# Performance work log

Hardware: AMD Instinct MI355X
Metric: run time of the kernel (lower is better)

Reference implementation:

```python
import jax, jax.numpy as jnp
import numpy as np

B, S, H = 8, 4096, 512

def setup_inputs() -> dict:
    key = jax.random.key(0)
    k1, k2 = jax.random.split(key)
    lstm_out = jax.random.normal(k1, (B, S, H), dtype=jnp.float32)
    W = jax.random.normal(k2, (2 * H, H), dtype=jnp.float32) * (1.0 / np.sqrt(H))
    b = jnp.zeros((2 * H,), dtype=jnp.float32)
    return {"lstm_out": lstm_out, "W": W, "b": b}

def reference(lstm_out, W, b):
    # noise_net: Linear(H, 2H) + Softplus
    noise = jax.nn.softplus(jnp.einsum('bsh,oh->bso', lstm_out, W) + b)  # [B,S,2H]
    Q = noise[:, :, :H]   # process noise
    R = noise[:, :, H:]   # observation noise

    def step(carry, inp):
        state, P = carry
        z, q, r = inp                      # each [B,H]
        P_pred = P + q
        K = P_pred / (P_pred + r + 1e-6)
        state = state + K * (z - state)
        P = (1.0 - K) * P_pred
        return (state, P), state

    state0 = lstm_out[:, 0, :]
    P0 = jnp.full_like(state0, 0.1)
    # time-major for scan: [S,B,H]
    xs = (jnp.swapaxes(lstm_out, 0, 1),
          jnp.swapaxes(Q, 0, 1),
          jnp.swapaxes(R, 0, 1))
    _, states = jax.lax.scan(step, (state0, P0), xs)  # [S,B,H]
    return jnp.swapaxes(states, 0, 1)  # [B,S,H]
```

## Files before the change

### kernel.cpp

```cpp
#include <hip/hip_runtime.h>
#include <hip/hip_bf16.h>

#define B_ 8
#define S_ 4096
#define H_ 512

using short8 = __attribute__((ext_vector_type(8))) short;
using f32x4  = __attribute__((ext_vector_type(4))) float;

__device__ __forceinline__ float bf2f(unsigned u16) {
    return __uint_as_float(u16 << 16);
}
__device__ __forceinline__ unsigned pk2bf(float x, float y) {
    __hip_bfloat162 h = __float22bfloat162_rn(make_float2(x, y));
    return *reinterpret_cast<unsigned*>(&h);
}
__device__ __forceinline__ float softplus_f(float x) {
    float sp = __logf(1.0f + __expf(x));
    return x > 15.0f ? x : sp;
}

typedef __attribute__((address_space(1))) void* gbl_ptr_t;
typedef __attribute__((address_space(3))) void* lds_ptr_t;
__device__ __forceinline__ void gload_lds16(const void* g, void* l) {
    __builtin_amdgcn_global_load_lds((gbl_ptr_t)g, (lds_ptr_t)l, 16, 0, 0);
}

#define ASZ8 2097152u
#define TOT8 2162688u

__global__ __launch_bounds__(256)
void convert_bf16(const float* __restrict__ A, const float* __restrict__ Wm,
                  uint4* __restrict__ Ab, uint4* __restrict__ Wb) {
    unsigned i = blockIdx.x * 256u + threadIdx.x;
    const float4* src; uint4* dst; unsigned off;
    if (i < ASZ8) { src = (const float4*)A;  dst = Ab; off = i; }
    else          { src = (const float4*)Wm; dst = Wb; off = i - ASZ8; }
    float4 a = src[2u * off], b = src[2u * off + 1u];
    uint4 o;
    o.x = pk2bf(a.x, a.y); o.y = pk2bf(a.z, a.w);
    o.z = pk2bf(b.x, b.y); o.w = pk2bf(b.z, b.w);
    dst[off] = o;
}

#define TM 128
#define TN 128
#define BK 64

__global__ __launch_bounds__(256)
void gemm_softplus(const unsigned short* __restrict__ Ab,
                   const unsigned short* __restrict__ Wb,
                   const float* __restrict__ bias,
                   unsigned* __restrict__ QR) {
    __shared__ unsigned short As[TM * BK];
    __shared__ unsigned short Bs[TN * BK];

    const int bid     = blockIdx.x;
    const int logical = (bid & 7) * 256 + (bid >> 3);
    const int bm = logical >> 3;
    const int bn = logical & 7;

    const int t    = threadIdx.x;
    const int wave = t >> 6;
    const int lane = t & 63;
    const int wm  = (wave >> 1) * 64;
    const int wn  = (wave & 1) * 64;
    const int l15 = lane & 15;
    const int l4  = lane >> 4;

    const int m0 = bm * TM;

    const int lr = lane >> 3;
    const int su = ((lane & 7) ^ lr) * 8;

    f32x4 acc[4][4] = {};

    for (int kc = 0; kc < 512; kc += BK) {
#pragma unroll
        for (int i = 0; i < 4; ++i) {
            const int j   = wave * 4 + i;
            const int row = j * 8 + lr;
            gload_lds16(Ab + (size_t)(m0 + row) * 512 + kc + su, &As[j * 512]);
            const int n = bn * 64 + (row & 31) + ((row & 64) >> 1) + ((row & 32) << 4);
            gload_lds16(Wb + (size_t)n * 512 + kc + su, &Bs[j * 512]);
        }
        __syncthreads();

#pragma unroll
        for (int kk = 0; kk < 2; ++kk) {
            short8 af[4], bf[4];
#pragma unroll
            for (int i = 0; i < 4; ++i) {
                const int ra = wm + i * 16 + l15;
                const int ua = ((kk * 4 + l4) ^ (ra & 7)) * 8;
                af[i] = *(const short8*)&As[ra * 64 + ua];
                const int rb = wn + i * 16 + l15;
                const int ub = ((kk * 4 + l4) ^ (rb & 7)) * 8;
                bf[i] = *(const short8*)&Bs[rb * 64 + ub];
            }
#pragma unroll
            for (int i = 0; i < 4; ++i)
#pragma unroll
                for (int j = 0; j < 4; ++j)
                    acc[i][j] = __builtin_amdgcn_mfma_f32_16x16x32_bf16(af[i], bf[j], acc[i][j], 0, 0, 0);
        }
        __syncthreads();
    }

#pragma unroll
    for (int j = 0; j < 2; ++j) {
        const int h  = bn * 64 + (wn >> 1) + j * 16 + l15;
        const float bq = bias[h];
        const float br = bias[h + 512];
#pragma unroll
        for (int i = 0; i < 4; ++i) {
            const int mb = m0 + wm + i * 16 + l4 * 4;
#pragma unroll
            for (int r = 0; r < 4; ++r) {
                const float qv = softplus_f(acc[i][j][r] + bq);
                const float rv = softplus_f(acc[i][j + 2][r] + br);
                QR[(size_t)(mb + r) * 512 + h] = pk2bf(qv, rv);
            }
        }
    }
}

#define CHUNK 64
#define WARM 64

__global__ __launch_bounds__(256)
void kalman_scan(const float* __restrict__ z,
                 const unsigned* __restrict__ QR,
                 float* __restrict__ out) {
    const int t     = threadIdx.x;
    const int b     = blockIdx.x & 7;
    const int chunk = blockIdx.x >> 3;
    const int h     = t * 2;
    const int s0    = chunk << 6;
    const int sw    = (chunk == 0) ? 0 : (s0 - WARM);
    const size_t base = ((size_t)(b * S_ + sw)) * 512 + h;

    const float2* zp  = (const float2*)(z + base);
    const uint2*  qrp = (const uint2*)(QR + base);
    float2*       op  = (float2*)(out + base);

    const int ng    = ((s0 + CHUNK) - sw) >> 3;
    const int skipg = (s0 - sw) >> 3;

    float2 Z0[8], Z1[8], Z2[8], Z3[8];
    uint2  Q0[8], Q1[8], Q2[8], Q3[8];

#define LOADG(g, Zb, Qb) { const int _o = (g) * 8;                          \
    _Pragma("unroll") for (int u = 0; u < 8; ++u) {                         \
        Zb[u] = zp[(_o + u) * 256]; Qb[u] = qrp[(_o + u) * 256]; } }

#define COMP(g, Zb, Qb) { const int _o = (g) * 8; const bool _st = (g) >= skipg; \
    _Pragma("unroll") for (int u = 0; u < 8; ++u) {                         \
        const unsigned qx = Qb[u].x, qy = Qb[u].y;                          \
        const float q0 = bf2f(qx & 0xffffu), r0 = bf2f(qx >> 16);           \
        const float q1 = bf2f(qy & 0xffffu), r1 = bf2f(qy >> 16);           \
        const float2 zv = Zb[u];                                            \
        const float Pp0 = P0 + q0, rr0 = r0 + 1e-6f;                        \
        const float K0  = Pp0 * __builtin_amdgcn_rcpf(Pp0 + rr0);           \
        st0 = fmaf(K0, zv.x - st0, st0); P0 = rr0 * K0;                     \
        const float Pp1 = P1 + q1, rr1 = r1 + 1e-6f;                        \
        const float K1  = Pp1 * __builtin_amdgcn_rcpf(Pp1 + rr1);           \
        st1 = fmaf(K1, zv.y - st1, st1); P1 = rr1 * K1;                     \
        if (_st) op[(_o + u) * 256] = make_float2(st0, st1); } }

    LOADG(0, Z0, Q0);
    LOADG(1, Z1, Q1);

    float st0 = Z0[0].x, st1 = Z0[0].y;
    float P0 = 0.1f, P1 = 0.1f;

    for (int gq = 0; gq < ng; gq += 4) {
        if (gq + 2 < ng) LOADG(gq + 2, Z2, Q2);
        COMP(gq, Z0, Q0);
        if (gq + 3 < ng) LOADG(gq + 3, Z3, Q3);
        COMP(gq + 1, Z1, Q1);
        if (gq + 4 < ng) LOADG(gq + 4, Z0, Q0);
        COMP(gq + 2, Z2, Q2);
        if (gq + 5 < ng) LOADG(gq + 5, Z1, Q1);
        COMP(gq + 3, Z3, Q3);
    }
#undef LOADG
#undef COMP
}

extern "C" void kernel_launch(void* const* d_in, const int* in_sizes, int n_in,
                              void* d_out, int out_size, void* d_ws, size_t ws_size,
                              hipStream_t stream) {
    const float* lstm = (const float*)d_in[0];
    const float* Wm   = (const float*)d_in[1];
    const float* bias = (const float*)d_in[2];
    float* out = (float*)d_out;

    unsigned* QRw = (unsigned*)d_ws;

    unsigned short* Abf = (unsigned short*)d_out;
    unsigned short* Wbf = (unsigned short*)((char*)d_out + (32u << 20));

    hipLaunchKernelGGL(convert_bf16, dim3(8448), dim3(256), 0, stream,
                       lstm, Wm, (uint4*)Abf, (uint4*)Wbf);

    hipLaunchKernelGGL(gemm_softplus, dim3(2048), dim3(256), 0, stream,
                       Abf, Wbf, bias, QRw);

    hipLaunchKernelGGL(kalman_scan, dim3(512), dim3(256), 0, stream,
                       lstm, QRw, out);
}
```

Baseline: 212.5 us.

## Double-buffer GEMM LDS loads, grid-stride convert, and restructure Kalman scan mapping

The GEMM now double-buffers its A/B tiles in LDS, prefetching the next K-slice with global_load_lds while computing the current one. It also uses explicit vmcnt/lgkmcnt waits, raw barriers, setprio around the MFMA bursts, and a min-blocks-per-CU hint of 2. The convert kernel becomes a grid-stride loop over 2048 blocks. The scan kernel now gives each thread one hidden element instead of two, splits H across two blocks, doubles the chunk length to 128 and deepens register prefetch to 8 groups, which trades less warm-up overhead for more registers and hand-managed synchronisation.

After: 201.2 us. 1.06x faster.

```diff
diff --git a/kernel.cpp b/kernel.cpp
--- a/kernel.cpp
+++ b/kernel.cpp
@@ -26,34 +26,42 @@
     __builtin_amdgcn_global_load_lds((gbl_ptr_t)g, (lds_ptr_t)l, 16, 0, 0);
 }
 
+#define BAR() do { asm volatile("" ::: "memory"); \
+                   __builtin_amdgcn_s_barrier(); \
+                   asm volatile("" ::: "memory"); } while (0)
+
+#define WAIT_LGKM0() do { asm volatile("s_waitcnt lgkmcnt(0)" ::: "memory"); \
+                          __builtin_amdgcn_sched_barrier(0); } while (0)
+
 #define ASZ8 2097152u
 #define TOT8 2162688u
 
 __global__ __launch_bounds__(256)
 void convert_bf16(const float* __restrict__ A, const float* __restrict__ Wm,
                   uint4* __restrict__ Ab, uint4* __restrict__ Wb) {
-    unsigned i = blockIdx.x * 256u + threadIdx.x;
-    const float4* src; uint4* dst; unsigned off;
-    if (i < ASZ8) { src = (const float4*)A;  dst = Ab; off = i; }
-    else          { src = (const float4*)Wm; dst = Wb; off = i - ASZ8; }
-    float4 a = src[2u * off], b = src[2u * off + 1u];
-    uint4 o;
-    o.x = pk2bf(a.x, a.y); o.y = pk2bf(a.z, a.w);
-    o.z = pk2bf(b.x, b.y); o.w = pk2bf(b.z, b.w);
-    dst[off] = o;
+    for (unsigned i = blockIdx.x * 256u + threadIdx.x; i < TOT8; i += 2048u * 256u) {
+        const float4* src; uint4* dst; unsigned off;
+        if (i < ASZ8) { src = (const float4*)A;  dst = Ab; off = i; }
+        else          { src = (const float4*)Wm; dst = Wb; off = i - ASZ8; }
+        float4 a = src[2u * off], b = src[2u * off + 1u];
+        uint4 o;
+        o.x = pk2bf(a.x, a.y); o.y = pk2bf(a.z, a.w);
+        o.z = pk2bf(b.x, b.y); o.w = pk2bf(b.z, b.w);
+        dst[off] = o;
+    }
 }
 
 #define TM 128
 #define TN 128
 #define BK 64
 
-__global__ __launch_bounds__(256)
+__global__ __launch_bounds__(256, 2)
 void gemm_softplus(const unsigned short* __restrict__ Ab,
                    const unsigned short* __restrict__ Wb,
                    const float* __restrict__ bias,
                    unsigned* __restrict__ QR) {
-    __shared__ unsigned short As[TM * BK];
-    __shared__ unsigned short Bs[TN * BK];
+    __shared__ unsigned short As[2][8192];
+    __shared__ unsigned short Bs[2][8192];
 
     const int bid     = blockIdx.x;
     const int logical = (bid & 7) * 256 + (bid >> 3);
@@ -73,39 +81,61 @@
     const int lr = lane >> 3;
     const int su = ((lane & 7) ^ lr) * 8;
 
+    const unsigned short* agp[4];
+    const unsigned short* bgp[4];
+    int ldsoff[4];
+#pragma unroll
+    for (int i = 0; i < 4; ++i) {
+        const int j   = wave * 4 + i;
+        const int row = j * 8 + lr;
+        agp[i] = Ab + (size_t)(m0 + row) * 512 + su;
+        const int n = bn * 64 + (row & 31) + ((row & 64) >> 1) + ((row & 32) << 4);
+        bgp[i] = Wb + (size_t)n * 512 + su;
+        ldsoff[i] = j * 512;
+    }
+
     f32x4 acc[4][4] = {};
 
-    for (int kc = 0; kc < 512; kc += BK) {
-#pragma unroll
-        for (int i = 0; i < 4; ++i) {
-            const int j   = wave * 4 + i;
-            const int row = j * 8 + lr;
-            gload_lds16(Ab + (size_t)(m0 + row) * 512 + kc + su, &As[j * 512]);
-            const int n = bn * 64 + (row & 31) + ((row & 64) >> 1) + ((row & 32) << 4);
-            gload_lds16(Wb + (size_t)n * 512 + kc + su, &Bs[j * 512]);
-        }
-        __syncthreads();
-
-#pragma unroll
-        for (int kk = 0; kk < 2; ++kk) {
-            short8 af[4], bf[4];
-#pragma unroll
-            for (int i = 0; i < 4; ++i) {
-                const int ra = wm + i * 16 + l15;
-                const int ua = ((kk * 4 + l4) ^ (ra & 7)) * 8;
-                af[i] = *(const short8*)&As[ra * 64 + ua];
-                const int rb = wn + i * 16 + l15;
-                const int ub = ((kk * 4 + l4) ^ (rb & 7)) * 8;
-                bf[i] = *(const short8*)&Bs[rb * 64 + ub];
-            }
-#pragma unroll
-            for (int i = 0; i < 4; ++i)
-#pragma unroll
-                for (int j = 0; j < 4; ++j)
-                    acc[i][j] = __builtin_amdgcn_mfma_f32_16x16x32_bf16(af[i], bf[j], acc[i][j], 0, 0, 0);
-        }
-        __syncthreads();
-    }
+#define STAGE(s) do { \
+    const int _sl = (s) & 1; const int _kc = (s) * BK; \
+    _Pragma("unroll") for (int i = 0; i < 4; ++i) { \
+        gload_lds16(agp[i] + _kc, &As[_sl][ldsoff[i]]); \
+        gload_lds16(bgp[i] + _kc, &Bs[_sl][ldsoff[i]]); \
+    } \
+} while (0)
+
+#define COMPUTE(g, VMN) do { \
+    const unsigned short* _a = &As[(g) & 1][0]; \
+    const unsigned short* _b = &Bs[(g) & 1][0]; \
+    asm volatile("s_waitcnt vmcnt(" #VMN ")" ::: "memory"); \
+    BAR(); \
+    _Pragma("unroll") for (int kk = 0; kk < 2; ++kk) { \
+        short8 af[4], bf[4]; \
+        _Pragma("unroll") for (int i = 0; i < 4; ++i) { \
+            const int ra = wm + i * 16 + l15; \
+            af[i] = *(const short8*)(_a + ra * 64 + (((kk * 4 + l4) ^ (ra & 7)) * 8)); \
+            const int rb = wn + i * 16 + l15; \
+            bf[i] = *(const short8*)(_b + rb * 64 + (((kk * 4 + l4) ^ (rb & 7)) * 8)); \
+        } \
+        WAIT_LGKM0(); \
+        __builtin_amdgcn_s_setprio(1); \
+        _Pragma("unroll") for (int i = 0; i < 4; ++i) \
+        _Pragma("unroll") for (int j = 0; j < 4; ++j) \
+            acc[i][j] = __builtin_amdgcn_mfma_f32_16x16x32_bf16(af[i], bf[j], acc[i][j], 0, 0, 0); \
+        __builtin_amdgcn_s_setprio(0); \
+    } \
+    BAR(); \
+} while (0)
+
+    STAGE(0);
+    for (int g = 0; g < 7; ++g) {
+        STAGE(g + 1);
+        COMPUTE(g, 8);
+    }
+    COMPUTE(7, 0);
+
+#undef COMPUTE
+#undef STAGE
 
 #pragma unroll
     for (int j = 0; j < 2; ++j) {
@@ -125,64 +155,59 @@
     }
 }
 
-#define CHUNK 64
+#define CHUNK 128
 #define WARM 64
 
-__global__ __launch_bounds__(256)
+__global__ __launch_bounds__(256, 2)
 void kalman_scan(const float* __restrict__ z,
                  const unsigned* __restrict__ QR,
                  float* __restrict__ out) {
     const int t     = threadIdx.x;
-    const int b     = blockIdx.x & 7;
-    const int chunk = blockIdx.x >> 3;
-    const int h     = t * 2;
-    const int s0    = chunk << 6;
+    const int hb    = blockIdx.x & 1;
+    const int b     = (blockIdx.x >> 1) & 7;
+    const int chunk = blockIdx.x >> 4;
+    const int h     = hb * 256 + t;
+    const int s0    = chunk << 7;
     const int sw    = (chunk == 0) ? 0 : (s0 - WARM);
     const size_t base = ((size_t)(b * S_ + sw)) * 512 + h;
 
-    const float2* zp  = (const float2*)(z + base);
-    const uint2*  qrp = (const uint2*)(QR + base);
-    float2*       op  = (float2*)(out + base);
+    const float*    zp  = z + base;
+    const unsigned* qrp = (const unsigned*)QR + base;
+    float*          op  = out + base;
 
     const int ng    = ((s0 + CHUNK) - sw) >> 3;
     const int skipg = (s0 - sw) >> 3;
 
-    float2 Z0[8], Z1[8], Z2[8], Z3[8];
-    uint2  Q0[8], Q1[8], Q2[8], Q3[8];
+    float    Z0[8], Z1[8], Z2[8], Z3[8], Z4[8], Z5[8], Z6[8], Z7[8];
+    unsigned Q0[8], Q1[8], Q2[8], Q3[8], Q4[8], Q5[8], Q6[8], Q7[8];
 
 #define LOADG(g, Zb, Qb) { const int _o = (g) * 8;                          \
     _Pragma("unroll") for (int u = 0; u < 8; ++u) {                         \
-        Zb[u] = zp[(_o + u) * 256]; Qb[u] = qrp[(_o + u) * 256]; } }
+        Zb[u] = zp[(size_t)(_o + u) * 512]; Qb[u] = qrp[(size_t)(_o + u) * 512]; } }
 
 #define COMP(g, Zb, Qb) { const int _o = (g) * 8; const bool _st = (g) >= skipg; \
     _Pragma("unroll") for (int u = 0; u < 8; ++u) {                         \
-        const unsigned qx = Qb[u].x, qy = Qb[u].y;                          \
-        const float q0 = bf2f(qx & 0xffffu), r0 = bf2f(qx >> 16);           \
-        const float q1 = bf2f(qy & 0xffffu), r1 = bf2f(qy >> 16);           \
-        const float2 zv = Zb[u];                                            \
-        const float Pp0 = P0 + q0, rr0 = r0 + 1e-6f;                        \
-        const float K0  = Pp0 * __builtin_amdgcn_rcpf(Pp0 + rr0);           \
-        st0 = fmaf(K0, zv.x - st0, st0); P0 = rr0 * K0;                     \
-        const float Pp1 = P1 + q1, rr1 = r1 + 1e-6f;                        \
-        const float K1  = Pp1 * __builtin_amdgcn_rcpf(Pp1 + rr1);           \
-        st1 = fmaf(K1, zv.y - st1, st1); P1 = rr1 * K1;                     \
-        if (_st) op[(_o + u) * 256] = make_float2(st0, st1); } }
-
-    LOADG(0, Z0, Q0);
-    LOADG(1, Z1, Q1);
-
-    float st0 = Z0[0].x, st1 = Z0[0].y;
-    float P0 = 0.1f, P1 = 0.1f;
-
-    for (int gq = 0; gq < ng; gq += 4) {
-        if (gq + 2 < ng) LOADG(gq + 2, Z2, Q2);
-        COMP(gq, Z0, Q0);
-        if (gq + 3 < ng) LOADG(gq + 3, Z3, Q3);
-        COMP(gq + 1, Z1, Q1);
-        if (gq + 4 < ng) LOADG(gq + 4, Z0, Q0);
-        COMP(gq + 2, Z2, Q2);
-        if (gq + 5 < ng) LOADG(gq + 5, Z1, Q1);
-        COMP(gq + 3, Z3, Q3);
+        const float q  = bf2f(Qb[u] & 0xffffu);                             \
+        const float r  = bf2f(Qb[u] >> 16);                                 \
+        const float Pp = P + q, rr = r + 1e-6f;                             \
+        const float K  = Pp * __builtin_amdgcn_rcpf(Pp + rr);               \
+        state = fmaf(K, Zb[u] - state, state); P = rr * K;                  \
+        if (_st) op[(size_t)(_o + u) * 512] = state; } }
+
+    LOADG(0, Z0, Q0); LOADG(1, Z1, Q1); LOADG(2, Z2, Q2); LOADG(3, Z3, Q3);
+
+    float state = Z0[0];
+    float P = 0.1f;
+
+    for (int g = 0; g < ng; g += 8) {
+        if (g + 4  < ng) LOADG(g + 4,  Z4, Q4); COMP(g,     Z0, Q0);
+        if (g + 5  < ng) LOADG(g + 5,  Z5, Q5); COMP(g + 1, Z1, Q1);
+        if (g + 6  < ng) LOADG(g + 6,  Z6, Q6); COMP(g + 2, Z2, Q2);
+        if (g + 7  < ng) LOADG(g + 7,  Z7, Q7); COMP(g + 3, Z3, Q3);
+        if (g + 8  < ng) LOADG(g + 8,  Z0, Q0); COMP(g + 4, Z4, Q4);
+        if (g + 9  < ng) LOADG(g + 9,  Z1, Q1); COMP(g + 5, Z5, Q5);
+        if (g + 10 < ng) LOADG(g + 10, Z2, Q2); COMP(g + 6, Z6, Q6);
+        if (g + 11 < ng) LOADG(g + 11, Z3, Q3); COMP(g + 7, Z7, Q7);
     }
 #undef LOADG
 #undef COMP
@@ -194,19 +219,18 @@
     const float* lstm = (const float*)d_in[0];
     const float* Wm   = (const float*)d_in[1];
     const float* bias = (const float*)d_in[2];
-    float* out = (float*)d_out;
 
     unsigned* QRw = (unsigned*)d_ws;
 
     unsigned short* Abf = (unsigned short*)d_out;
     unsigned short* Wbf = (unsigned short*)((char*)d_out + (32u << 20));
 
-    hipLaunchKernelGGL(convert_bf16, dim3(8448), dim3(256), 0, stream,
+    hipLaunchKernelGGL(convert_bf16, dim3(2048), dim3(256), 0, stream,
                        lstm, Wm, (uint4*)Abf, (uint4*)Wbf);
 
     hipLaunchKernelGGL(gemm_softplus, dim3(2048), dim3(256), 0, stream,
                        Abf, Wbf, bias, QRw);
 
     hipLaunchKernelGGL(kalman_scan, dim3(512), dim3(256), 0, stream,
-                       lstm, QRw, out);
-}
+                       lstm, QRw, (float*)d_out);
+}
```
